# Kernel tuning notes

Measured on AMD Instinct MI355X. Metric: run time of the kernel, lower is better.

## Reference

```python
import jax, jax.numpy as jnp
import numpy as np

N = 1_000_000
B = 64            # number of point clouds (segments)
IN_DIM = 3
HID = 128
AFF = 16
AH = 64           # agent hidden
AL = 32           # agent latent
AA = 8            # agent action


def setup_inputs() -> dict:
    key = jax.random.key(0)
    ks = jax.random.split(key, 20)
    s = 0.05
    inp = {
        "pos": jax.random.normal(ks[0], (N, IN_DIM), jnp.float32),
        "batch": jnp.sort(jax.random.randint(ks[1], (N,), 0, B, jnp.int32)),
        "agent_h": jnp.zeros((B, AH), jnp.float32),
        "coherence_signal_prev": jnp.zeros((B, 1), jnp.float32),
        "coherence_spatial_prev": jnp.zeros((N,), jnp.float32),
        # FunctorF params (3 -> 128 -> 16)
        "Wf1": jax.random.normal(ks[2], (IN_DIM, HID), jnp.float32) * s,
        "bf1": jnp.zeros((HID,), jnp.float32),
        "Wf2": jax.random.normal(ks[3], (HID, AFF), jnp.float32) * s,
        "bf2": jnp.zeros((AFF,), jnp.float32),
        # FunctorG params (16 -> 128 -> 3)
        "Wg1": jax.random.normal(ks[4], (AFF, HID), jnp.float32) * s,
        "bg1": jnp.zeros((HID,), jnp.float32),
        "Wg2": jax.random.normal(ks[5], (HID, IN_DIM), jnp.float32) * s,
        "bg2": jnp.zeros((IN_DIM,), jnp.float32),
        # AgentC GRU cell (obs=16 -> h=64) + latent/action heads
        "Wx": jax.random.normal(ks[6], (AFF, 3 * AH), jnp.float32) * s,
        "Wh": jax.random.normal(ks[7], (AH, 3 * AH), jnp.float32) * s,
        "bx": jnp.zeros((3 * AH,), jnp.float32),
        "bh": jnp.zeros((3 * AH,), jnp.float32),
        "Wlat": jax.random.normal(ks[8], (AH, AL), jnp.float32) * s,
        "blat": jnp.zeros((AL,), jnp.float32),
        "Wact": jax.random.normal(ks[9], (AL, AA), jnp.float32) * s,
        "bact": jnp.zeros((AA,), jnp.float32),
    }
    return inp


def _segment_mean(x, seg, num_segments):
    # x: (N, ...) float; seg: (N,) int. Mean over each segment (empty -> 0).
    sums = jax.ops.segment_sum(x, seg, num_segments=num_segments)
    counts = jax.ops.segment_sum(jnp.ones_like(seg, x.dtype), seg, num_segments=num_segments)
    denom = jnp.maximum(counts, 1.0)
    return sums / (denom[:, None] if x.ndim > 1 else denom)


def _forward(pos, batch, agent_h, Wf1, bf1, Wf2, bf2, Wg1, bg1, Wg2, bg2,
             Wx, Wh, bx, bh, Wlat, blat, Wact, bact):
    # F: Shape -> Affordance (per-point MLP)
    affordances = jax.nn.relu(pos @ Wf1 + bf1) @ Wf2 + bf2              # (N, AFF)
    # G: Affordance -> Shape reconstruction
    reconstructed_pos = jax.nn.relu(affordances @ Wg1 + bg1) @ Wg2 + bg2  # (N, 3)
    # Coherence (eta): per-point squared error, segment-mean per cloud
    point_errors = jnp.sum((pos - reconstructed_pos) ** 2, axis=-1)     # (N,)
    coherence_signal = _segment_mean(point_errors, batch, B)[:, None]   # (B, 1)
    coherence_spatial = point_errors                                    # (N,)
    # Segment-mean pooled affordances per cloud
    batch_affordances = _segment_mean(affordances, batch, B)            # (B, AFF)
    # AgentC: GRU cell + latent/action heads
    gx = batch_affordances @ Wx + bx                                    # (B, 3*AH)
    gh = agent_h @ Wh + bh                                              # (B, 3*AH)
    gx_r, gx_z, gx_n = jnp.split(gx, 3, axis=-1)
    gh_r, gh_z, gh_n = jnp.split(gh, 3, axis=-1)
    r = jax.nn.sigmoid(gx_r + gh_r)
    z = jax.nn.sigmoid(gx_z + gh_z)
    n = jnp.tanh(gx_n + r * gh_n)
    agent_h_next = (1.0 - z) * n + z * agent_h                          # (B, AH)
    latent = jnp.tanh(agent_h_next @ Wlat + blat)                       # (B, AL)
    agent_action = latent @ Wact + bact                                 # (B, AA)
    return (affordances, reconstructed_pos, coherence_signal,
            coherence_spatial, agent_action, agent_h_next)


def reference(pos, batch, agent_h, coherence_signal_prev, coherence_spatial_prev,
              Wf1, bf1, Wf2, bf2, Wg1, bg1, Wg2, bg2,
              Wx, Wh, bx, bh, Wlat, blat, Wact, bact):
    # coherence_*_prev are part of the original interface but unused in the math.
    return _forward(pos, batch, agent_h, Wf1, bf1, Wf2, bf2, Wg1, bg1, Wg2, bg2,
                    Wx, Wh, bx, bh, Wlat, blat, Wact, bact)
```

## Files before the change

### kernel.cpp

```cpp
#include <hip/hip_runtime.h>
#include <stdint.h>

#define N_PTS 1000000
#define B_SEG 64
#define HID 128
#define AFFD 16
#define AH 64
#define AL 32
#define AA 8

#define TPB 256
#define NT 16
#define PTS_WAVE (16 * NT)
#define PTS_BLK (PTS_WAVE * 4)

#define O_AFF 0
#define O_REC (16 * N_PTS)
#define O_SIG (19 * N_PTS)
#define O_SPA (19 * N_PTS + B_SEG)
#define O_ACT (20 * N_PTS + B_SEG)
#define O_HN  (20 * N_PTS + B_SEG + B_SEG * AA)


typedef __attribute__((ext_vector_type(8))) short bf16x8;
typedef __attribute__((ext_vector_type(4))) float f32x4;

static __device__ __forceinline__ short f2bf(float f) {
  __bf16 b = (__bf16)f;
  return __builtin_bit_cast(short, b);
}

__global__ __launch_bounds__(TPB, 1) void point_kernel(
    const float* __restrict__ pos, const int* __restrict__ batch,
    const float* __restrict__ Wf1, const float* __restrict__ bf1v,
    const float* __restrict__ Wf2, const float* __restrict__ bf2v,
    const float* __restrict__ Wg1, const float* __restrict__ bg1v,
    const float* __restrict__ Wg2, const float* __restrict__ bg2v,
    float* __restrict__ out, float* __restrict__ ws) {
  const int lane = threadIdx.x & 63;
  const int wid = threadIdx.x >> 6;
  const int m = lane & 15;
  const int q = lane >> 4;
  const int wbase = blockIdx.x * PTS_BLK + wid * PTS_WAVE;

  bf16x8 Af1[8], Ag1[8], Af2[4], Ag2[4];
#pragma unroll
  for (int jb = 0; jb < 8; jb++) {
    const int j = jb * 16 + m;
    bf16x8 a = {0, 0, 0, 0, 0, 0, 0, 0};
    if (q == 0) {
      a[0] = f2bf(Wf1[0 * HID + j]);
      a[1] = f2bf(Wf1[1 * HID + j]);
      a[2] = f2bf(Wf1[2 * HID + j]);
      a[3] = f2bf(bf1v[j]);
    }
    Af1[jb] = a;
    bf16x8 g = {0, 0, 0, 0, 0, 0, 0, 0};
#pragma unroll
    for (int e = 0; e < 4; e++) g[e] = f2bf(Wg1[(4 * q + e) * HID + j]);
    if (q == 0) g[4] = f2bf(bg1v[j]);
    Ag1[jb] = g;
  }
#pragma unroll
  for (int kb = 0; kb < 4; kb++) {
    bf16x8 a2, g2;
#pragma unroll
    for (int e = 0; e < 8; e++) {
      const int j = kb * 32 + 4 * q + (e & 3) + 16 * (e >> 2);
      a2[e] = f2bf(Wf2[j * AFFD + m]);
      g2[e] = (m < 3) ? f2bf(Wg2[j * 3 + m]) : (short)0;
    }
    Af2[kb] = a2;
    Ag2[kb] = g2;
  }
  const float bf2r0 = bf2v[4 * q + 0], bf2r1 = bf2v[4 * q + 1];
  const float bf2r2 = bf2v[4 * q + 2], bf2r3 = bf2v[4 * q + 3];
  const float bg20 = bg2v[0], bg21 = bg2v[1], bg22 = bg2v[2];
  const short one = (short)0x3F80;
  const f32x4 zf = {0.f, 0.f, 0.f, 0.f};

  int cur = -1, cntT = 0;
  float accA0 = 0.f, accA1 = 0.f, accA2 = 0.f, accA3 = 0.f, accE = 0.f;

  auto flush = [&]() {
    float r0 = accA0, r1 = accA1, r2 = accA2, r3 = accA3, re = accE;
#pragma unroll
    for (int msk = 1; msk <= 8; msk <<= 1) {
      r0 += __shfl_xor(r0, msk);
      r1 += __shfl_xor(r1, msk);
      r2 += __shfl_xor(r2, msk);
      r3 += __shfl_xor(r3, msk);
      re += __shfl_xor(re, msk);
    }
    if (m == 0) {
      float* wp = ws + cur * 18;
      atomicAdd(wp + 2 + 4 * q + 0, r0);
      atomicAdd(wp + 2 + 4 * q + 1, r1);
      atomicAdd(wp + 2 + 4 * q + 2, r2);
      atomicAdd(wp + 2 + 4 * q + 3, r3);
      if (q == 0) {
        atomicAdd(wp + 0, re);
        atomicAdd(wp + 1, 16.f * (float)cntT);
      }
    }
    accA0 = accA1 = accA2 = accA3 = accE = 0.f;
    cntT = 0;
  };

#pragma unroll 1
  for (int t = 0; t < NT; t++) {
    const int pt0 = wbase + t * 16;
    const int p = pt0 + m;
    const bool v = (p < N_PTS);
    const int pc = v ? p : (N_PTS - 1);
    const float x = pos[pc * 3 + 0], y = pos[pc * 3 + 1], z = pos[pc * 3 + 2];
    const int sg = batch[pc];

    bf16x8 Bp = {0, 0, 0, 0, 0, 0, 0, 0};
    if (q == 0) {
      Bp[0] = f2bf(x);
      Bp[1] = f2bf(y);
      Bp[2] = f2bf(z);
      Bp[3] = one;
    }

    bf16x8 Bh[4];
#pragma unroll
    for (int kb = 0; kb < 4; kb++) {
      f32x4 c0 = __builtin_amdgcn_mfma_f32_16x16x32_bf16(Af1[2 * kb + 0], Bp, zf, 0, 0, 0);
      f32x4 c1 = __builtin_amdgcn_mfma_f32_16x16x32_bf16(Af1[2 * kb + 1], Bp, zf, 0, 0, 0);
      bf16x8 b;
      b[0] = f2bf(fmaxf(c0[0], 0.f));
      b[1] = f2bf(fmaxf(c0[1], 0.f));
      b[2] = f2bf(fmaxf(c0[2], 0.f));
      b[3] = f2bf(fmaxf(c0[3], 0.f));
      b[4] = f2bf(fmaxf(c1[0], 0.f));
      b[5] = f2bf(fmaxf(c1[1], 0.f));
      b[6] = f2bf(fmaxf(c1[2], 0.f));
      b[7] = f2bf(fmaxf(c1[3], 0.f));
      Bh[kb] = b;
    }

    f32x4 Ca = zf;
#pragma unroll
    for (int kb = 0; kb < 4; kb++)
      Ca = __builtin_amdgcn_mfma_f32_16x16x32_bf16(Af2[kb], Bh[kb], Ca, 0, 0, 0);
    const float a0 = Ca[0] + bf2r0, a1 = Ca[1] + bf2r1;
    const float a2 = Ca[2] + bf2r2, a3 = Ca[3] + bf2r3;

    bf16x8 Ba;
    Ba[0] = f2bf(a0);
    Ba[1] = f2bf(a1);
    Ba[2] = f2bf(a2);
    Ba[3] = f2bf(a3);
    Ba[4] = one;
    Ba[5] = 0;
    Ba[6] = 0;
    Ba[7] = 0;

    bf16x8 Bh2[4];
#pragma unroll
    for (int kb = 0; kb < 4; kb++) {
      f32x4 c0 = __builtin_amdgcn_mfma_f32_16x16x32_bf16(Ag1[2 * kb + 0], Ba, zf, 0, 0, 0);
      f32x4 c1 = __builtin_amdgcn_mfma_f32_16x16x32_bf16(Ag1[2 * kb + 1], Ba, zf, 0, 0, 0);
      bf16x8 b;
      b[0] = f2bf(fmaxf(c0[0], 0.f));
      b[1] = f2bf(fmaxf(c0[1], 0.f));
      b[2] = f2bf(fmaxf(c0[2], 0.f));
      b[3] = f2bf(fmaxf(c0[3], 0.f));
      b[4] = f2bf(fmaxf(c1[0], 0.f));
      b[5] = f2bf(fmaxf(c1[1], 0.f));
      b[6] = f2bf(fmaxf(c1[2], 0.f));
      b[7] = f2bf(fmaxf(c1[3], 0.f));
      Bh2[kb] = b;
    }

    f32x4 Cr = zf;
#pragma unroll
    for (int kb = 0; kb < 4; kb++)
      Cr = __builtin_amdgcn_mfma_f32_16x16x32_bf16(Ag2[kb], Bh2[kb], Cr, 0, 0, 0);

    float err = 0.f, rc0 = 0.f, rc1 = 0.f, rc2 = 0.f;
    if (q == 0) {
      rc0 = Cr[0] + bg20;
      rc1 = Cr[1] + bg21;
      rc2 = Cr[2] + bg22;
      const float dx = x - rc0, dy = y - rc1, dz = z - rc2;
      err = fmaf(dx, dx, fmaf(dy, dy, dz * dz));
    }

    if (v) {
      float4 st;
      st.x = a0; st.y = a1; st.z = a2; st.w = a3;
      *(float4*)(out + O_AFF + (size_t)p * 16 + 4 * q) = st;
      if (q == 0) {
        float* orc = out + O_REC + (size_t)p * 3;
        orc[0] = rc0; orc[1] = rc1; orc[2] = rc2;
        out[O_SPA + p] = err;
      }
    }

    const int useg = __shfl(sg, 0);
    const bool clean = __all(sg == useg) && (pt0 + 16 <= N_PTS);
    if (clean && useg == cur) {
      accA0 += a0; accA1 += a1; accA2 += a2; accA3 += a3;
      accE += err;
      cntT++;
    } else {
      if (cntT > 0) flush();
      if (clean) {
        cur = useg;
        accA0 = a0; accA1 = a1; accA2 = a2; accA3 = a3;
        accE = err;
        cntT = 1;
      } else {
        cur = -1;
        if (v) {
          float* wp = ws + sg * 18;
          atomicAdd(wp + 2 + 4 * q + 0, a0);
          atomicAdd(wp + 2 + 4 * q + 1, a1);
          atomicAdd(wp + 2 + 4 * q + 2, a2);
          atomicAdd(wp + 2 + 4 * q + 3, a3);
          if (q == 0) {
            atomicAdd(wp + 0, err);
            atomicAdd(wp + 1, 1.f);
          }
        }
      }
    }
  }
  if (cntT > 0) flush();
}

__global__ __launch_bounds__(64) void agent_kernel(
    const float* __restrict__ ws, const float* __restrict__ agent_h,
    const float* __restrict__ Wx, const float* __restrict__ Wh,
    const float* __restrict__ bx, const float* __restrict__ bh,
    const float* __restrict__ Wlat, const float* __restrict__ blat,
    const float* __restrict__ Wact, const float* __restrict__ bact,
    float* __restrict__ out) {
  const int b = blockIdx.x;
  const int t = threadIdx.x;
  __shared__ float sAff[AFFD];
  __shared__ float sHn[AH];
  __shared__ float sLat[AL];

  const float cnt = fmaxf(ws[b * 18 + 1], 1.f);
  if (t == 0) out[O_SIG + b] = ws[b * 18 + 0] / cnt;
  if (t < AFFD) sAff[t] = ws[b * 18 + 2 + t] / cnt;
  const float h_prev = agent_h[b * AH + t];
  __syncthreads();

  float pr  = bx[t] + bh[t];
  float pz  = bx[64 + t] + bh[64 + t];
  float pnx = bx[128 + t];
  float pnh = bh[128 + t];
#pragma unroll
  for (int k = 0; k < AFFD; k++) {
    const float a = sAff[k];
    pr  = fmaf(a, Wx[k * 192 + t], pr);
    pz  = fmaf(a, Wx[k * 192 + 64 + t], pz);
    pnx = fmaf(a, Wx[k * 192 + 128 + t], pnx);
  }
#pragma unroll
  for (int k = 0; k < AH; k++) {
    const float h = __shfl(h_prev, k);
    pr  = fmaf(h, Wh[k * 192 + t], pr);
    pz  = fmaf(h, Wh[k * 192 + 64 + t], pz);
    pnh = fmaf(h, Wh[k * 192 + 128 + t], pnh);
  }
  const float r = 1.f / (1.f + expf(-pr));
  const float z = 1.f / (1.f + expf(-pz));
  const float n = tanhf(pnx + r * pnh);
  const float hn = fmaf(1.f - z, n, z * h_prev);
  sHn[t] = hn;
  out[O_HN + b * AH + t] = hn;
  __syncthreads();

  if (t < AL) {
    float acc = blat[t];
#pragma unroll
    for (int k = 0; k < AH; k++) acc = fmaf(sHn[k], Wlat[k * AL + t], acc);
    sLat[t] = tanhf(acc);
  }
  __syncthreads();

  if (t < AA) {
    float acc = bact[t];
#pragma unroll
    for (int k = 0; k < AL; k++) acc = fmaf(sLat[k], Wact[k * AA + t], acc);
    out[O_ACT + b * AA + t] = acc;
  }
}

extern "C" void kernel_launch(void* const* d_in, const int* in_sizes, int n_in,
                              void* d_out, int out_size, void* d_ws, size_t ws_size,
                              hipStream_t stream) {
  const float* pos     = (const float*)d_in[0];
  const int*   batch   = (const int*)d_in[1];
  const float* agent_h = (const float*)d_in[2];
  const float* Wf1  = (const float*)d_in[5];
  const float* bf1v = (const float*)d_in[6];
  const float* Wf2  = (const float*)d_in[7];
  const float* bf2v = (const float*)d_in[8];
  const float* Wg1  = (const float*)d_in[9];
  const float* bg1v = (const float*)d_in[10];
  const float* Wg2  = (const float*)d_in[11];
  const float* bg2v = (const float*)d_in[12];
  const float* Wx   = (const float*)d_in[13];
  const float* Wh   = (const float*)d_in[14];
  const float* bx   = (const float*)d_in[15];
  const float* bh   = (const float*)d_in[16];
  const float* Wlat = (const float*)d_in[17];
  const float* blat = (const float*)d_in[18];
  const float* Wact = (const float*)d_in[19];
  const float* bact = (const float*)d_in[20];
  float* out = (float*)d_out;
  float* ws = (float*)d_ws;

  hipMemsetAsync(ws, 0, B_SEG * 18 * sizeof(float), stream);

  const int nblk = (N_PTS + PTS_BLK - 1) / PTS_BLK;
  point_kernel<<<nblk, TPB, 0, stream>>>(pos, batch, Wf1, bf1v, Wf2, bf2v,
                                         Wg1, bg1v, Wg2, bg2v, out, ws);
  agent_kernel<<<B_SEG, 64, 0, stream>>>(ws, agent_h, Wx, Wh, bx, bh,
                                         Wlat, blat, Wact, bact, out);
}
```

Before: 222.4 us.

## Interleave two point tiles, replicate atomic workspace, fast path for single-segment waves

Processes two 16-point tiles per iteration, splitting each accumulating MFMA chain into two independent chains for more instruction-level parallelism. Halves points per wave, which doubles the number of blocks. Adds a whole-wave clean-segment fast path that skips per-tile ballot checks and flushes once at the end. Spreads atomics across up to 8 replicated workspace copies to cut contention, at the cost of a larger memset and a reduction loop in the agent kernel.

```diff
diff --git a/kernel.cpp b/kernel.cpp
--- a/kernel.cpp
+++ b/kernel.cpp
@@ -10,9 +10,10 @@
 #define AA 8
 
 #define TPB 256
-#define NT 16
+#define NT 8
 #define PTS_WAVE (16 * NT)
 #define PTS_BLK (PTS_WAVE * 4)
+#define MAX_REP 8
 
 #define O_AFF 0
 #define O_REC (16 * N_PTS)
@@ -36,12 +37,13 @@
     const float* __restrict__ Wf2, const float* __restrict__ bf2v,
     const float* __restrict__ Wg1, const float* __restrict__ bg1v,
     const float* __restrict__ Wg2, const float* __restrict__ bg2v,
-    float* __restrict__ out, float* __restrict__ ws) {
+    float* __restrict__ out, float* __restrict__ ws, int rep) {
   const int lane = threadIdx.x & 63;
   const int wid = threadIdx.x >> 6;
   const int m = lane & 15;
   const int q = lane >> 4;
   const int wbase = blockIdx.x * PTS_BLK + wid * PTS_WAVE;
+  float* __restrict__ wsr = ws + (size_t)(blockIdx.x % rep) * (B_SEG * 18);
 
   bf16x8 Af1[8], Ag1[8], Af2[4], Ag2[4];
 #pragma unroll
@@ -80,10 +82,10 @@
   const f32x4 zf = {0.f, 0.f, 0.f, 0.f};
 
   int cur = -1, cntT = 0;
-  float accA0 = 0.f, accA1 = 0.f, accA2 = 0.f, accA3 = 0.f, accE = 0.f;
+  float acc0 = 0.f, acc1 = 0.f, acc2 = 0.f, acc3 = 0.f, accE = 0.f;
 
   auto flush = [&]() {
-    float r0 = accA0, r1 = accA1, r2 = accA2, r3 = accA3, re = accE;
+    float r0 = acc0, r1 = acc1, r2 = acc2, r3 = acc3, re = accE;
 #pragma unroll
     for (int msk = 1; msk <= 8; msk <<= 1) {
       r0 += __shfl_xor(r0, msk);
@@ -93,7 +95,7 @@
       re += __shfl_xor(re, msk);
     }
     if (m == 0) {
-      float* wp = ws + cur * 18;
+      float* wp = wsr + cur * 18;
       atomicAdd(wp + 2 + 4 * q + 0, r0);
       atomicAdd(wp + 2 + 4 * q + 1, r1);
       atomicAdd(wp + 2 + 4 * q + 2, r2);
@@ -103,137 +105,193 @@
         atomicAdd(wp + 1, 16.f * (float)cntT);
       }
     }
-    accA0 = accA1 = accA2 = accA3 = accE = 0.f;
+    acc0 = acc1 = acc2 = acc3 = accE = 0.f;
     cntT = 0;
   };
 
+  auto do_pair = [&](int pt0, float (&aa)[2][4], float (&ee)[2], int (&sgv)[2],
+                     bool (&vv)[2]) {
+    float X[2], Y[2], Z[2];
+    bf16x8 Bp[2];
+#pragma unroll
+    for (int u = 0; u < 2; u++) {
+      const int p = pt0 + 16 * u + m;
+      vv[u] = (p < N_PTS);
+      const int pc = vv[u] ? p : (N_PTS - 1);
+      X[u] = pos[pc * 3 + 0];
+      Y[u] = pos[pc * 3 + 1];
+      Z[u] = pos[pc * 3 + 2];
+      sgv[u] = batch[pc];
+      bf16x8 b = {0, 0, 0, 0, 0, 0, 0, 0};
+      if (q == 0) {
+        b[0] = f2bf(X[u]);
+        b[1] = f2bf(Y[u]);
+        b[2] = f2bf(Z[u]);
+        b[3] = one;
+      }
+      Bp[u] = b;
+    }
+
+    bf16x8 Bh[2][4];
+#pragma unroll
+    for (int u = 0; u < 2; u++)
+#pragma unroll
+      for (int kb = 0; kb < 4; kb++) {
+        f32x4 c0 = __builtin_amdgcn_mfma_f32_16x16x32_bf16(Af1[2 * kb + 0], Bp[u], zf, 0, 0, 0);
+        f32x4 c1 = __builtin_amdgcn_mfma_f32_16x16x32_bf16(Af1[2 * kb + 1], Bp[u], zf, 0, 0, 0);
+        bf16x8 b;
+        b[0] = f2bf(fmaxf(c0[0], 0.f));
+        b[1] = f2bf(fmaxf(c0[1], 0.f));
+        b[2] = f2bf(fmaxf(c0[2], 0.f));
+        b[3] = f2bf(fmaxf(c0[3], 0.f));
+        b[4] = f2bf(fmaxf(c1[0], 0.f));
+        b[5] = f2bf(fmaxf(c1[1], 0.f));
+        b[6] = f2bf(fmaxf(c1[2], 0.f));
+        b[7] = f2bf(fmaxf(c1[3], 0.f));
+        Bh[u][kb] = b;
+      }
+
+    bf16x8 Ba[2];
+#pragma unroll
+    for (int u = 0; u < 2; u++) {
+      f32x4 c01 = __builtin_amdgcn_mfma_f32_16x16x32_bf16(Af2[0], Bh[u][0], zf, 0, 0, 0);
+      c01 = __builtin_amdgcn_mfma_f32_16x16x32_bf16(Af2[1], Bh[u][1], c01, 0, 0, 0);
+      f32x4 c23 = __builtin_amdgcn_mfma_f32_16x16x32_bf16(Af2[2], Bh[u][2], zf, 0, 0, 0);
+      c23 = __builtin_amdgcn_mfma_f32_16x16x32_bf16(Af2[3], Bh[u][3], c23, 0, 0, 0);
+      aa[u][0] = c01[0] + c23[0] + bf2r0;
+      aa[u][1] = c01[1] + c23[1] + bf2r1;
+      aa[u][2] = c01[2] + c23[2] + bf2r2;
+      aa[u][3] = c01[3] + c23[3] + bf2r3;
+      bf16x8 b;
+      b[0] = f2bf(aa[u][0]);
+      b[1] = f2bf(aa[u][1]);
+      b[2] = f2bf(aa[u][2]);
+      b[3] = f2bf(aa[u][3]);
+      b[4] = one;
+      b[5] = 0;
+      b[6] = 0;
+      b[7] = 0;
+      Ba[u] = b;
+    }
+
+    bf16x8 Bh2[2][4];
+#pragma unroll
+    for (int u = 0; u < 2; u++)
+#pragma unroll
+      for (int kb = 0; kb < 4; kb++) {
+        f32x4 c0 = __builtin_amdgcn_mfma_f32_16x16x32_bf16(Ag1[2 * kb + 0], Ba[u], zf, 0, 0, 0);
+        f32x4 c1 = __builtin_amdgcn_mfma_f32_16x16x32_bf16(Ag1[2 * kb + 1], Ba[u], zf, 0, 0, 0);
+        bf16x8 b;
+        b[0] = f2bf(fmaxf(c0[0], 0.f));
+        b[1] = f2bf(fmaxf(c0[1], 0.f));
+        b[2] = f2bf(fmaxf(c0[2], 0.f));
+        b[3] = f2bf(fmaxf(c0[3], 0.f));
+        b[4] = f2bf(fmaxf(c1[0], 0.f));
+        b[5] = f2bf(fmaxf(c1[1], 0.f));
+        b[6] = f2bf(fmaxf(c1[2], 0.f));
+        b[7] = f2bf(fmaxf(c1[3], 0.f));
+        Bh2[u][kb] = b;
+      }
+
+#pragma unroll
+    for (int u = 0; u < 2; u++) {
+      f32x4 c01 = __builtin_amdgcn_mfma_f32_16x16x32_bf16(Ag2[0], Bh2[u][0], zf, 0, 0, 0);
+      c01 = __builtin_amdgcn_mfma_f32_16x16x32_bf16(Ag2[1], Bh2[u][1], c01, 0, 0, 0);
+      f32x4 c23 = __builtin_amdgcn_mfma_f32_16x16x32_bf16(Ag2[2], Bh2[u][2], zf, 0, 0, 0);
+      c23 = __builtin_amdgcn_mfma_f32_16x16x32_bf16(Ag2[3], Bh2[u][3], c23, 0, 0, 0);
+
+      float err = 0.f, rc0 = 0.f, rc1 = 0.f, rc2 = 0.f;
+      if (q == 0) {
+        rc0 = c01[0] + c23[0] + bg20;
+        rc1 = c01[1] + c23[1] + bg21;
+        rc2 = c01[2] + c23[2] + bg22;
+        const float dx = X[u] - rc0, dy = Y[u] - rc1, dz = Z[u] - rc2;
+        err = fmaf(dx, dx, fmaf(dy, dy, dz * dz));
+      }
+      ee[u] = err;
+
+      if (vv[u]) {
+        const int p = pt0 + 16 * u + m;
+        float4 st;
+        st.x = aa[u][0]; st.y = aa[u][1]; st.z = aa[u][2]; st.w = aa[u][3];
+        *(float4*)(out + O_AFF + (size_t)p * 16 + 4 * q) = st;
+        if (q == 0) {
+          float* orc = out + O_REC + (size_t)p * 3;
+          orc[0] = rc0; orc[1] = rc1; orc[2] = rc2;
+          out[O_SPA + p] = err;
+        }
+      }
+    }
+  };
+
+  const int cA = (wbase < N_PTS) ? wbase : (N_PTS - 1);
+  const int cB = (wbase + PTS_WAVE - 1 < N_PTS) ? (wbase + PTS_WAVE - 1) : (N_PTS - 1);
+  const int segFirst = batch[cA];
+  const bool wave_clean = (wbase + PTS_WAVE <= N_PTS) && (segFirst == batch[cB]);
+
+  float aa[2][4];
+  float ee[2];
+  int sgv[2];
+  bool vv[2];
+
+  if (wave_clean) {
 #pragma unroll 1
-  for (int t = 0; t < NT; t++) {
-    const int pt0 = wbase + t * 16;
-    const int p = pt0 + m;
-    const bool v = (p < N_PTS);
-    const int pc = v ? p : (N_PTS - 1);
-    const float x = pos[pc * 3 + 0], y = pos[pc * 3 + 1], z = pos[pc * 3 + 2];
-    const int sg = batch[pc];
-
-    bf16x8 Bp = {0, 0, 0, 0, 0, 0, 0, 0};
-    if (q == 0) {
-      Bp[0] = f2bf(x);
-      Bp[1] = f2bf(y);
-      Bp[2] = f2bf(z);
-      Bp[3] = one;
-    }
-
-    bf16x8 Bh[4];
-#pragma unroll
-    for (int kb = 0; kb < 4; kb++) {
-      f32x4 c0 = __builtin_amdgcn_mfma_f32_16x16x32_bf16(Af1[2 * kb + 0], Bp, zf, 0, 0, 0);
-      f32x4 c1 = __builtin_amdgcn_mfma_f32_16x16x32_bf16(Af1[2 * kb + 1], Bp, zf, 0, 0, 0);
-      bf16x8 b;
-      b[0] = f2bf(fmaxf(c0[0], 0.f));
-      b[1] = f2bf(fmaxf(c0[1], 0.f));
-      b[2] = f2bf(fmaxf(c0[2], 0.f));
-      b[3] = f2bf(fmaxf(c0[3], 0.f));
-      b[4] = f2bf(fmaxf(c1[0], 0.f));
-      b[5] = f2bf(fmaxf(c1[1], 0.f));
-      b[6] = f2bf(fmaxf(c1[2], 0.f));
-      b[7] = f2bf(fmaxf(c1[3], 0.f));
-      Bh[kb] = b;
-    }
-
-    f32x4 Ca = zf;
-#pragma unroll
-    for (int kb = 0; kb < 4; kb++)
-      Ca = __builtin_amdgcn_mfma_f32_16x16x32_bf16(Af2[kb], Bh[kb], Ca, 0, 0, 0);
-    const float a0 = Ca[0] + bf2r0, a1 = Ca[1] + bf2r1;
-    const float a2 = Ca[2] + bf2r2, a3 = Ca[3] + bf2r3;
-
-    bf16x8 Ba;
-    Ba[0] = f2bf(a0);
-    Ba[1] = f2bf(a1);
-    Ba[2] = f2bf(a2);
-    Ba[3] = f2bf(a3);
-    Ba[4] = one;
-    Ba[5] = 0;
-    Ba[6] = 0;
-    Ba[7] = 0;
-
-    bf16x8 Bh2[4];
-#pragma unroll
-    for (int kb = 0; kb < 4; kb++) {
-      f32x4 c0 = __builtin_amdgcn_mfma_f32_16x16x32_bf16(Ag1[2 * kb + 0], Ba, zf, 0, 0, 0);
-      f32x4 c1 = __builtin_amdgcn_mfma_f32_16x16x32_bf16(Ag1[2 * kb + 1], Ba, zf, 0, 0, 0);
-      bf16x8 b;
-      b[0] = f2bf(fmaxf(c0[0], 0.f));
-      b[1] = f2bf(fmaxf(c0[1], 0.f));
-      b[2] = f2bf(fmaxf(c0[2], 0.f));
-      b[3] = f2bf(fmaxf(c0[3], 0.f));
-      b[4] = f2bf(fmaxf(c1[0], 0.f));
-      b[5] = f2bf(fmaxf(c1[1], 0.f));
-      b[6] = f2bf(fmaxf(c1[2], 0.f));
-      b[7] = f2bf(fmaxf(c1[3], 0.f));
-      Bh2[kb] = b;
-    }
-
-    f32x4 Cr = zf;
-#pragma unroll
-    for (int kb = 0; kb < 4; kb++)
-      Cr = __builtin_amdgcn_mfma_f32_16x16x32_bf16(Ag2[kb], Bh2[kb], Cr, 0, 0, 0);
-
-    float err = 0.f, rc0 = 0.f, rc1 = 0.f, rc2 = 0.f;
-    if (q == 0) {
-      rc0 = Cr[0] + bg20;
-      rc1 = Cr[1] + bg21;
-      rc2 = Cr[2] + bg22;
-      const float dx = x - rc0, dy = y - rc1, dz = z - rc2;
-      err = fmaf(dx, dx, fmaf(dy, dy, dz * dz));
-    }
-
-    if (v) {
-      float4 st;
-      st.x = a0; st.y = a1; st.z = a2; st.w = a3;
-      *(float4*)(out + O_AFF + (size_t)p * 16 + 4 * q) = st;
-      if (q == 0) {
-        float* orc = out + O_REC + (size_t)p * 3;
-        orc[0] = rc0; orc[1] = rc1; orc[2] = rc2;
-        out[O_SPA + p] = err;
-      }
-    }
-
-    const int useg = __shfl(sg, 0);
-    const bool clean = __all(sg == useg) && (pt0 + 16 <= N_PTS);
-    if (clean && useg == cur) {
-      accA0 += a0; accA1 += a1; accA2 += a2; accA3 += a3;
-      accE += err;
-      cntT++;
-    } else {
-      if (cntT > 0) flush();
-      if (clean) {
-        cur = useg;
-        accA0 = a0; accA1 = a1; accA2 = a2; accA3 = a3;
-        accE = err;
-        cntT = 1;
-      } else {
-        cur = -1;
-        if (v) {
-          float* wp = ws + sg * 18;
-          atomicAdd(wp + 2 + 4 * q + 0, a0);
-          atomicAdd(wp + 2 + 4 * q + 1, a1);
-          atomicAdd(wp + 2 + 4 * q + 2, a2);
-          atomicAdd(wp + 2 + 4 * q + 3, a3);
-          if (q == 0) {
-            atomicAdd(wp + 0, err);
-            atomicAdd(wp + 1, 1.f);
+    for (int tt = 0; tt < NT; tt += 2) {
+      do_pair(wbase + tt * 16, aa, ee, sgv, vv);
+      acc0 += aa[0][0] + aa[1][0];
+      acc1 += aa[0][1] + aa[1][1];
+      acc2 += aa[0][2] + aa[1][2];
+      acc3 += aa[0][3] + aa[1][3];
+      accE += ee[0] + ee[1];
+    }
+    cur = segFirst;
+    cntT = NT;
+    flush();
+  } else {
+#pragma unroll 1
+    for (int tt = 0; tt < NT; tt += 2) {
+      do_pair(wbase + tt * 16, aa, ee, sgv, vv);
+#pragma unroll
+      for (int u = 0; u < 2; u++) {
+        const int pt0u = wbase + (tt + u) * 16;
+        const int useg = __shfl(sgv[u], 0);
+        const bool cln = __all(sgv[u] == useg) && (pt0u + 16 <= N_PTS);
+        if (cln && useg == cur) {
+          acc0 += aa[u][0]; acc1 += aa[u][1];
+          acc2 += aa[u][2]; acc3 += aa[u][3];
+          accE += ee[u];
+          cntT++;
+        } else {
+          if (cntT > 0) flush();
+          if (cln) {
+            cur = useg;
+            acc0 = aa[u][0]; acc1 = aa[u][1];
+            acc2 = aa[u][2]; acc3 = aa[u][3];
+            accE = ee[u];
+            cntT = 1;
+          } else {
+            cur = -1;
+            if (vv[u]) {
+              float* wp = wsr + sgv[u] * 18;
+              atomicAdd(wp + 2 + 4 * q + 0, aa[u][0]);
+              atomicAdd(wp + 2 + 4 * q + 1, aa[u][1]);
+              atomicAdd(wp + 2 + 4 * q + 2, aa[u][2]);
+              atomicAdd(wp + 2 + 4 * q + 3, aa[u][3]);
+              if (q == 0) {
+                atomicAdd(wp + 0, ee[u]);
+                atomicAdd(wp + 1, 1.f);
+              }
+            }
           }
         }
       }
     }
-  }
-  if (cntT > 0) flush();
+    if (cntT > 0) flush();
+  }
 }
 
 __global__ __launch_bounds__(64) void agent_kernel(
-    const float* __restrict__ ws, const float* __restrict__ agent_h,
+    const float* __restrict__ ws, int rep, const float* __restrict__ agent_h,
     const float* __restrict__ Wx, const float* __restrict__ Wh,
     const float* __restrict__ bx, const float* __restrict__ bh,
     const float* __restrict__ Wlat, const float* __restrict__ blat,
@@ -245,9 +303,16 @@
   __shared__ float sHn[AH];
   __shared__ float sLat[AL];
 
-  const float cnt = fmaxf(ws[b * 18 + 1], 1.f);
-  if (t == 0) out[O_SIG + b] = ws[b * 18 + 0] / cnt;
-  if (t < AFFD) sAff[t] = ws[b * 18 + 2 + t] / cnt;
+  float errs = 0.f, cnts = 0.f, affs = 0.f;
+  for (int r = 0; r < rep; r++) {
+    const float* wp = ws + ((size_t)r * B_SEG + b) * 18;
+    errs += wp[0];
+    cnts += wp[1];
+    if (t < AFFD) affs += wp[2 + t];
+  }
+  const float cnt = fmaxf(cnts, 1.f);
+  if (t == 0) out[O_SIG + b] = errs / cnt;
+  if (t < AFFD) sAff[t] = affs / cnt;
   const float h_prev = agent_h[b * AH + t];
   __syncthreads();
 
@@ -318,11 +383,16 @@
   float* out = (float*)d_out;
   float* ws = (float*)d_ws;
 
-  hipMemsetAsync(ws, 0, B_SEG * 18 * sizeof(float), stream);
+  const size_t one_rep = (size_t)B_SEG * 18 * sizeof(float);
+  int rep = (int)(ws_size / one_rep);
+  if (rep > MAX_REP) rep = MAX_REP;
+  if (rep < 1) rep = 1;
+
+  hipMemsetAsync(ws, 0, (size_t)rep * one_rep, stream);
 
   const int nblk = (N_PTS + PTS_BLK - 1) / PTS_BLK;
   point_kernel<<<nblk, TPB, 0, stream>>>(pos, batch, Wf1, bf1v, Wf2, bf2v,
-                                         Wg1, bg1v, Wg2, bg2v, out, ws);
-  agent_kernel<<<B_SEG, 64, 0, stream>>>(ws, agent_h, Wx, Wh, bx, bh,
+                                         Wg1, bg1v, Wg2, bg2v, out, ws, rep);
+  agent_kernel<<<B_SEG, 64, 0, stream>>>(ws, rep, agent_h, Wx, Wh, bx, bh,
                                          Wlat, blat, Wact, bact, out);
 }
```

Result: slower. 228.4 us (+2.7%).
